# Kernel tuning notes

Measured on AMD Instinct MI355X. Metric: run time of the kernel, lower is better.

The kernel has to match this reference:

```python
import jax, jax.numpy as jnp
import numpy as np

KERNEL = 3
PAD = KERNEL // 2


def _conv1x1(x, w, b):
    # x: [B,C,H,W], w: [O,C], b: [O]
    return jnp.einsum('bchw,oc->bohw', x, w) + b[None, :, None, None]


def setup_inputs() -> dict:
    key = jax.random.key(0)
    ks = jax.random.split(key, 8)
    B, C, H, W = 4, 64, 512, 512
    MID = 32
    s = lambda k, shape, scale=0.05: jax.random.normal(k, shape, dtype=jnp.float32) * scale
    return {
        'x': jax.random.normal(ks[0], (B, C, H, W), dtype=jnp.float32),
        'w1': s(ks[1], (MID, C)),
        'b1': s(ks[2], (MID,)),
        'w2': s(ks[3], (MID, C)),
        'b2': s(ks[4], (MID,)),
        'w3': s(ks[5], (C, C)),
        'b3': s(ks[6], (C,)),
        'gamma': s(ks[7], (1,), 1.0),
    }


def reference(x, w1, b1, w2, b2, w3, b3, gamma):
    B, C, H, W = x.shape
    x1 = _conv1x1(x, w1, b1)   # [B,32,H,W]
    x2 = _conv1x1(x, w2, b2)   # [B,32,H,W]
    x3 = _conv1x1(x, w3, b3)   # [B,C,H,W]
    pad = ((0, 0), (0, 0), (PAD, PAD), (PAD, PAD))
    x1p = jnp.pad(x1, pad)
    x3p = jnp.pad(x3, pad)
    g = gamma[0]
    out = x
    for i in range(KERNEL):
        for j in range(KERNEL):
            x1s = x1p[:, :, i:i + H, j:j + W]
            x3s = x3p[:, :, i:i + H, j:j + W]
            # sigmoid elementwise, then sum over mid channels -> [B,1,H,W]
            attn = jax.nn.sigmoid(x2 * x1s).sum(axis=1, keepdims=True)
            out = out + g * x3s * attn
    return out
```

## Files before the change

### kernel.cpp

```cpp
#include <hip/hip_runtime.h>
#include <hip/hip_bf16.h>

#define HH 512
#define WW 512
#define HWSZ (512 * 512)
#define CIN 64
#define MID 32

#define TS 16
#define HC 18
#define NCOL (HC * HC)
#define X1STRIDE 17

__device__ __forceinline__ unsigned f2bf(float v) {
    unsigned u = __float_as_uint(v);
    return (u + 0x7fffu + ((u >> 16) & 1u)) >> 16;
}

__global__ __launch_bounds__(256, 2)
void fused_local_attn(const float* __restrict__ x,
                      const float* __restrict__ w1, const float* __restrict__ b1,
                      const float* __restrict__ w2, const float* __restrict__ b2,
                      const float* __restrict__ w3, const float* __restrict__ b3,
                      const float* __restrict__ gamma,
                      float* __restrict__ out)
{
    __shared__ unsigned sX1[NCOL * X1STRIDE];

    const int tid = threadIdx.x;
    const int lx = tid & 15, ly = tid >> 4;
    const int b  = blockIdx.z;
    const int w0 = blockIdx.x * TS, h0 = blockIdx.y * TS;
    const int hh = h0 + ly, ww = w0 + lx;

    const float* xb = x + (size_t)b * CIN * HWSZ;

    for (int cidx = tid; cidx < NCOL; cidx += 256) {
        int sy = cidx / HC;
        int sx = cidx - sy * HC;
        int gh = h0 - 1 + sy, gw = w0 - 1 + sx;
        bool valid = (gh >= 0) && (gh < HH) && (gw >= 0) && (gw < WW);
        float acc[MID];
#pragma unroll
        for (int oc = 0; oc < MID; ++oc) acc[oc] = valid ? b1[oc] : 0.f;
        if (valid) {
            const float* xp = xb + gh * WW + gw;
#pragma unroll 4
            for (int ic = 0; ic < CIN; ++ic) {
                float xv = xp[(size_t)ic * HWSZ];
#pragma unroll
                for (int oc = 0; oc < MID; ++oc) acc[oc] += w1[oc * CIN + ic] * xv;
            }
        }
#pragma unroll
        for (int p = 0; p < MID / 2; ++p)
            sX1[cidx * X1STRIDE + p] = f2bf(acc[2 * p]) | (f2bf(acc[2 * p + 1]) << 16);
    }
    __syncthreads();

    float x2n[MID];
#pragma unroll
    for (int oc = 0; oc < MID; ++oc) x2n[oc] = b2[oc];
    {
        const float* xp = xb + hh * WW + ww;
#pragma unroll 4
        for (int ic = 0; ic < CIN; ++ic) {
            float xv = xp[(size_t)ic * HWSZ];
#pragma unroll
            for (int oc = 0; oc < MID; ++oc) x2n[oc] += w2[oc * CIN + ic] * xv;
        }
    }
#pragma unroll
    for (int oc = 0; oc < MID; ++oc) x2n[oc] *= -1.4426950408889634f;

    float S[9];
    float T = 0.f;
#pragma unroll
    for (int dy = 0; dy < 3; ++dy) {
#pragma unroll
        for (int dx = 0; dx < 3; ++dx) {
            int j = dy * 3 + dx;
            int gh = hh - 1 + dy, gw = ww - 1 + dx;
            float s = 0.f;
            if ((gh >= 0) && (gh < HH) && (gw >= 0) && (gw < WW)) {
                int col = (ly + dy) * HC + (lx + dx);
                const unsigned* xp1 = &sX1[col * X1STRIDE];
#pragma unroll
                for (int p = 0; p < MID / 2; ++p) {
                    unsigned u = xp1[p];
                    float lo = __uint_as_float(u << 16);
                    float hi = __uint_as_float(u & 0xffff0000u);
                    float t0 = x2n[2 * p] * lo;
                    float t1 = x2n[2 * p + 1] * hi;
                    s += __builtin_amdgcn_rcpf(1.f + exp2f(t0));
                    s += __builtin_amdgcn_rcpf(1.f + exp2f(t1));
                }
            }
            S[j] = s;
            T += s;
        }
    }

    int off[9];
#pragma unroll
    for (int dy = 0; dy < 3; ++dy) {
        int gh = hh - 1 + dy;
        gh = gh < 0 ? 0 : (gh > HH - 1 ? HH - 1 : gh);
#pragma unroll
        for (int dx = 0; dx < 3; ++dx) {
            int gw = ww - 1 + dx;
            gw = gw < 0 ? 0 : (gw > WW - 1 ? WW - 1 : gw);
            off[dy * 3 + dx] = gh * WW + gw;
        }
    }
    float y[CIN];
#pragma unroll 8
    for (int ic = 0; ic < CIN; ++ic) {
        const float* xp = xb + (size_t)ic * HWSZ;
        float a = 0.f;
#pragma unroll
        for (int j = 0; j < 9; ++j) a += S[j] * xp[off[j]];
        y[ic] = a;
    }

    const float g = gamma[0];
    const float* xp = xb + hh * WW + ww;
    float* op = out + (size_t)b * CIN * HWSZ + hh * WW + ww;
#pragma unroll 2
    for (int c = 0; c < CIN; ++c) {
        float acc = b3[c] * T;
#pragma unroll
        for (int ic = 0; ic < CIN; ++ic) acc += w3[c * CIN + ic] * y[ic];
        op[(size_t)c * HWSZ] = xp[(size_t)c * HWSZ] + g * acc;
    }
}

extern "C" void kernel_launch(void* const* d_in, const int* in_sizes, int n_in,
                              void* d_out, int out_size, void* d_ws, size_t ws_size,
                              hipStream_t stream) {
    const float* x     = (const float*)d_in[0];
    const float* w1    = (const float*)d_in[1];
    const float* b1    = (const float*)d_in[2];
    const float* w2    = (const float*)d_in[3];
    const float* b2    = (const float*)d_in[4];
    const float* w3    = (const float*)d_in[5];
    const float* b3    = (const float*)d_in[6];
    const float* gamma = (const float*)d_in[7];
    float* out = (float*)d_out;

    dim3 grid(WW / TS, HH / TS, 4);
    fused_local_attn<<<grid, dim3(256), 0, stream>>>(x, w1, b1, w2, b2, w3, b3, gamma, out);
}
```

Baseline: 1.250 ms.

## Compute x3 in shared memory per tile instead of applying w3 after attention sum

Each thread now computes x1 and x2 for its own pixel, plus x3 as a full 64-channel conv, and stores bf16 x1 and x3 in shared memory. Only halo threads compute the border columns. The output is then a weighted sum of the neighbouring x3 values read from shared memory, which replaces the 9-tap gather of x from global memory followed by a 64x64 matvec. This avoids the per-pixel global neighbour loads and removes the redundant x1 recompute in the interior. In exchange it needs a much larger LDS buffer (about 65KB, which may limit occupancy), leaves only 68 threads doing serial halo work, and rounds x3 to bf16, which costs precision.

```diff
diff --git a/kernel.cpp b/kernel.cpp
--- a/kernel.cpp
+++ b/kernel.cpp
@@ -10,11 +10,18 @@
 #define TS 16
 #define HC 18
 #define NCOL (HC * HC)
-#define X1STRIDE 17
+#define CSTR 25
 
-__device__ __forceinline__ unsigned f2bf(float v) {
-    unsigned u = __float_as_uint(v);
-    return (u + 0x7fffu + ((u >> 16) & 1u)) >> 16;
+__device__ __forceinline__ unsigned pack_bf2(float a, float b) {
+    __hip_bfloat162 h = __float22bfloat162_rn(float2{a, b});
+    unsigned u;
+    __builtin_memcpy(&u, &h, 4);
+    return u;
+}
+__device__ __forceinline__ float bflo(unsigned u) { return __uint_as_float(u << 16); }
+__device__ __forceinline__ float bfhi(unsigned u) { return __uint_as_float(u & 0xffff0000u); }
+__device__ __forceinline__ float sigm_t(float t) {
+    return __builtin_amdgcn_rcpf(1.f + __builtin_amdgcn_exp2f(t));
 }
 
 __global__ __launch_bounds__(256, 2)
@@ -25,7 +32,7 @@
                       const float* __restrict__ gamma,
                       float* __restrict__ out)
 {
-    __shared__ unsigned sX1[NCOL * X1STRIDE];
+    __shared__ uint2 sT[NCOL * CSTR];
 
     const int tid = threadIdx.x;
     const int lx = tid & 15, ly = tid >> 4;
@@ -34,105 +41,128 @@
     const int hh = h0 + ly, ww = w0 + lx;
 
     const float* xb = x + (size_t)b * CIN * HWSZ;
+    const float* xp = xb + hh * WW + ww;
 
-    for (int cidx = tid; cidx < NCOL; cidx += 256) {
-        int sy = cidx / HC;
-        int sx = cidx - sy * HC;
-        int gh = h0 - 1 + sy, gw = w0 - 1 + sx;
-        bool valid = (gh >= 0) && (gh < HH) && (gw >= 0) && (gw < WW);
-        float acc[MID];
+    const int colo = (ly + 1) * HC + (lx + 1);
+    float x2n[MID];
+    {
+        float a1[MID], a2[MID];
 #pragma unroll
-        for (int oc = 0; oc < MID; ++oc) acc[oc] = valid ? b1[oc] : 0.f;
-        if (valid) {
-            const float* xp = xb + gh * WW + gw;
-#pragma unroll 4
-            for (int ic = 0; ic < CIN; ++ic) {
-                float xv = xp[(size_t)ic * HWSZ];
-#pragma unroll
-                for (int oc = 0; oc < MID; ++oc) acc[oc] += w1[oc * CIN + ic] * xv;
-            }
-        }
-#pragma unroll
-        for (int p = 0; p < MID / 2; ++p)
-            sX1[cidx * X1STRIDE + p] = f2bf(acc[2 * p]) | (f2bf(acc[2 * p + 1]) << 16);
-    }
-    __syncthreads();
-
-    float x2n[MID];
-#pragma unroll
-    for (int oc = 0; oc < MID; ++oc) x2n[oc] = b2[oc];
-    {
-        const float* xp = xb + hh * WW + ww;
+        for (int oc = 0; oc < MID; ++oc) { a1[oc] = b1[oc]; a2[oc] = b2[oc]; }
 #pragma unroll 4
         for (int ic = 0; ic < CIN; ++ic) {
             float xv = xp[(size_t)ic * HWSZ];
 #pragma unroll
-            for (int oc = 0; oc < MID; ++oc) x2n[oc] += w2[oc * CIN + ic] * xv;
+            for (int oc = 0; oc < MID; ++oc) {
+                a1[oc] += w1[oc * CIN + ic] * xv;
+                a2[oc] += w2[oc * CIN + ic] * xv;
+            }
         }
+        uint2* p1 = &sT[colo * CSTR];
+#pragma unroll
+        for (int p = 0; p < 8; ++p)
+            p1[p] = uint2{pack_bf2(a1[4 * p], a1[4 * p + 1]),
+                          pack_bf2(a1[4 * p + 2], a1[4 * p + 3])};
+#pragma unroll
+        for (int oc = 0; oc < MID; ++oc) x2n[oc] = a2[oc] * -1.4426950408889634f;
     }
+    {
+        float a3[CIN];
 #pragma unroll
-    for (int oc = 0; oc < MID; ++oc) x2n[oc] *= -1.4426950408889634f;
+        for (int c = 0; c < CIN; ++c) a3[c] = b3[c];
+#pragma unroll 4
+        for (int ic = 0; ic < CIN; ++ic) {
+            float xv = xp[(size_t)ic * HWSZ];
+#pragma unroll
+            for (int c = 0; c < CIN; ++c) a3[c] += w3[c * CIN + ic] * xv;
+        }
+        uint2* p3 = &sT[colo * CSTR + 8];
+#pragma unroll
+        for (int p = 0; p < 16; ++p)
+            p3[p] = uint2{pack_bf2(a3[4 * p], a3[4 * p + 1]),
+                          pack_bf2(a3[4 * p + 2], a3[4 * p + 3])};
+    }
+
+    if (tid < 68) {
+        int sy, sx;
+        if (tid < 18)      { sy = 0;        sx = tid; }
+        else if (tid < 36) { sy = 17;       sx = tid - 18; }
+        else if (tid < 52) { sy = tid - 35; sx = 0; }
+        else               { sy = tid - 51; sx = 17; }
+        const int col = sy * HC + sx;
+        const int gh = h0 - 1 + sy, gw = w0 - 1 + sx;
+        const bool valid = (gh >= 0) && (gh < HH) && (gw >= 0) && (gw < WW);
+        float a1[MID], a3[CIN];
+#pragma unroll
+        for (int oc = 0; oc < MID; ++oc) a1[oc] = valid ? b1[oc] : 0.f;
+#pragma unroll
+        for (int c = 0; c < CIN; ++c) a3[c] = valid ? b3[c] : 0.f;
+        if (valid) {
+            const float* xq = xb + gh * WW + gw;
+#pragma unroll 4
+            for (int ic = 0; ic < CIN; ++ic) {
+                float xv = xq[(size_t)ic * HWSZ];
+#pragma unroll
+                for (int oc = 0; oc < MID; ++oc) a1[oc] += w1[oc * CIN + ic] * xv;
+#pragma unroll
+                for (int c = 0; c < CIN; ++c) a3[c] += w3[c * CIN + ic] * xv;
+            }
+        }
+        uint2* p1 = &sT[col * CSTR];
+#pragma unroll
+        for (int p = 0; p < 8; ++p)
+            p1[p] = uint2{pack_bf2(a1[4 * p], a1[4 * p + 1]),
+                          pack_bf2(a1[4 * p + 2], a1[4 * p + 3])};
+        uint2* p3 = &sT[col * CSTR + 8];
+#pragma unroll
+        for (int p = 0; p < 16; ++p)
+            p3[p] = uint2{pack_bf2(a3[4 * p], a3[4 * p + 1]),
+                          pack_bf2(a3[4 * p + 2], a3[4 * p + 3])};
+    }
+    __syncthreads();
 
     float S[9];
-    float T = 0.f;
 #pragma unroll
-    for (int dy = 0; dy < 3; ++dy) {
+    for (int j = 0; j < 9; ++j) {
+        const int dy = j / 3, dx = j % 3;
+        const int col = (ly + dy) * HC + (lx + dx);
+        const uint2* q = &sT[col * CSTR];
+        float s = 0.f;
 #pragma unroll
-        for (int dx = 0; dx < 3; ++dx) {
-            int j = dy * 3 + dx;
-            int gh = hh - 1 + dy, gw = ww - 1 + dx;
-            float s = 0.f;
-            if ((gh >= 0) && (gh < HH) && (gw >= 0) && (gw < WW)) {
-                int col = (ly + dy) * HC + (lx + dx);
-                const unsigned* xp1 = &sX1[col * X1STRIDE];
+        for (int p = 0; p < 8; ++p) {
+            uint2 u = q[p];
+            s += sigm_t(x2n[4 * p]     * bflo(u.x));
+            s += sigm_t(x2n[4 * p + 1] * bfhi(u.x));
+            s += sigm_t(x2n[4 * p + 2] * bflo(u.y));
+            s += sigm_t(x2n[4 * p + 3] * bfhi(u.y));
+        }
+        S[j] = s;
+    }
+
+    float acc[CIN];
 #pragma unroll
-                for (int p = 0; p < MID / 2; ++p) {
-                    unsigned u = xp1[p];
-                    float lo = __uint_as_float(u << 16);
-                    float hi = __uint_as_float(u & 0xffff0000u);
-                    float t0 = x2n[2 * p] * lo;
-                    float t1 = x2n[2 * p + 1] * hi;
-                    s += __builtin_amdgcn_rcpf(1.f + exp2f(t0));
-                    s += __builtin_amdgcn_rcpf(1.f + exp2f(t1));
-                }
-            }
-            S[j] = s;
-            T += s;
+    for (int c = 0; c < CIN; ++c) acc[c] = 0.f;
+#pragma unroll
+    for (int j = 0; j < 9; ++j) {
+        const int dy = j / 3, dx = j % 3;
+        const int col = (ly + dy) * HC + (lx + dx);
+        const float Sj = S[j];
+        const uint2* q = &sT[col * CSTR + 8];
+#pragma unroll
+        for (int t = 0; t < 16; ++t) {
+            uint2 u = q[t];
+            acc[4 * t]     += Sj * bflo(u.x);
+            acc[4 * t + 1] += Sj * bfhi(u.x);
+            acc[4 * t + 2] += Sj * bflo(u.y);
+            acc[4 * t + 3] += Sj * bfhi(u.y);
         }
     }
 
-    int off[9];
-#pragma unroll
-    for (int dy = 0; dy < 3; ++dy) {
-        int gh = hh - 1 + dy;
-        gh = gh < 0 ? 0 : (gh > HH - 1 ? HH - 1 : gh);
-#pragma unroll
-        for (int dx = 0; dx < 3; ++dx) {
-            int gw = ww - 1 + dx;
-            gw = gw < 0 ? 0 : (gw > WW - 1 ? WW - 1 : gw);
-            off[dy * 3 + dx] = gh * WW + gw;
-        }
-    }
-    float y[CIN];
-#pragma unroll 8
-    for (int ic = 0; ic < CIN; ++ic) {
-        const float* xp = xb + (size_t)ic * HWSZ;
-        float a = 0.f;
-#pragma unroll
-        for (int j = 0; j < 9; ++j) a += S[j] * xp[off[j]];
-        y[ic] = a;
-    }
-
     const float g = gamma[0];
-    const float* xp = xb + hh * WW + ww;
     float* op = out + (size_t)b * CIN * HWSZ + hh * WW + ww;
-#pragma unroll 2
-    for (int c = 0; c < CIN; ++c) {
-        float acc = b3[c] * T;
-#pragma unroll
-        for (int ic = 0; ic < CIN; ++ic) acc += w3[c * CIN + ic] * y[ic];
-        op[(size_t)c * HWSZ] = xp[(size_t)c * HWSZ] + g * acc;
-    }
+#pragma unroll 4
+    for (int c = 0; c < CIN; ++c)
+        op[(size_t)c * HWSZ] = xp[(size_t)c * HWSZ] + g * acc[c];
 }
 
 extern "C" void kernel_launch(void* const* d_in, const int* in_sizes, int n_in,
```

New measurement: 3.189 ms. +155.0%, slower.
